# Kernel optimization log

Measured on AMD Instinct MI355X. Metric: run time of the kernel, lower is better.

## Reference

```python
import jax, jax.numpy as jnp
import numpy as np

EPS = 1e-6
H = 12  # heads

def layernorm(x, alpha, bias):
    # Faithful to source: unbiased std (ddof=1) and division by (std + eps)
    mean = jnp.mean(x, axis=-1, keepdims=True)
    std = jnp.std(x, axis=-1, ddof=1, keepdims=True)
    return alpha * (x - mean) / (std + EPS) + bias

def setup_inputs() -> dict:
    key = jax.random.key(0)
    ks = jax.random.split(key, 8)
    B, S, D, F = 2, 2048, 768, 3072
    w_scale = 0.02  # keep activations in a sane range
    return {
        "x": jax.random.normal(ks[0], (B, S, D), dtype=jnp.float32),
        "src_mask": jnp.ones((B, 1, 1, S), dtype=jnp.int32),
        "wq": jax.random.normal(ks[1], (D, D), dtype=jnp.float32) * w_scale,
        "wk": jax.random.normal(ks[2], (D, D), dtype=jnp.float32) * w_scale,
        "wv": jax.random.normal(ks[3], (D, D), dtype=jnp.float32) * w_scale,
        "wo": jax.random.normal(ks[4], (D, D), dtype=jnp.float32) * w_scale,
        "w1": jax.random.normal(ks[5], (D, F), dtype=jnp.float32) * w_scale,
        "b1": jnp.zeros((F,), dtype=jnp.float32),
        "w2": jax.random.normal(ks[6], (F, D), dtype=jnp.float32) * w_scale,
        "b2": jnp.zeros((D,), dtype=jnp.float32),
        "ln1_alpha": jnp.ones((1,), dtype=jnp.float32),
        "ln1_bias": jnp.zeros((1,), dtype=jnp.float32),
        "ln2_alpha": jnp.ones((1,), dtype=jnp.float32),
        "ln2_bias": jnp.zeros((1,), dtype=jnp.float32),
    }

def reference(x, src_mask, wq, wk, wv, wo, w1, b1, w2, b2,
              ln1_alpha, ln1_bias, ln2_alpha, ln2_bias):
    B, S, D = x.shape
    dk = D // H
    # ---- residual 1: pre-LN self-attention ----
    t = layernorm(x, ln1_alpha, ln1_bias)
    q = (t @ wq).reshape(B, S, H, dk).transpose(0, 2, 1, 3)  # [B,H,S,dk]
    k = (t @ wk).reshape(B, S, H, dk).transpose(0, 2, 1, 3)
    v = (t @ wv).reshape(B, S, H, dk).transpose(0, 2, 1, 3)
    scores = jnp.einsum('bhqd,bhkd->bhqk', q, k) / jnp.sqrt(jnp.float32(dk))
    # Faithful to source quirk: masked positions are SET to 1e-9 (not -inf)
    scores = jnp.where(src_mask == 0, jnp.float32(1e-9), scores)
    attn = jax.nn.softmax(scores, axis=-1)
    o = jnp.einsum('bhqk,bhkd->bhqd', attn, v)
    o = o.transpose(0, 2, 1, 3).reshape(B, S, D) @ wo
    x = x + o
    # ---- residual 2: pre-LN FFN ----
    t = layernorm(x, ln2_alpha, ln2_bias)
    ffn = jax.nn.relu(t @ w1 + b1) @ w2 + b2
    return x + ffn
```

## Files before the change

### kernel.cpp

```cpp
#include <hip/hip_runtime.h>

typedef float f32x4 __attribute__((ext_vector_type(4)));
typedef __bf16 bf16x8 __attribute__((ext_vector_type(8)));

__device__ __forceinline__ unsigned short f2bf(float f) {
    union { float f; unsigned u; } v; v.f = f;
    unsigned r = v.u + 0x7fffu + ((v.u >> 16) & 1u);
    return (unsigned short)(r >> 16);
}

#define AS1 __attribute__((address_space(1)))
#define AS3 __attribute__((address_space(3)))
__device__ __forceinline__ void async16(const void* g, void* l) {
    __builtin_amdgcn_global_load_lds((AS1 void*)g, (AS3 void*)l, 16, 0, 0);
}

__device__ __forceinline__ void sync_lds() {
    asm volatile("s_waitcnt lgkmcnt(0)\n\ts_barrier" ::: "memory");
}

#define SWZ4(r) ((((r) & 3) ^ (((r) >> 2) & 3)))

__global__ void transpose_cvt(const float* __restrict__ W, unsigned short* __restrict__ Wt,
                              int K, int N) {
    __shared__ float tile[32][33];
    int n0 = blockIdx.x * 32, k0 = blockIdx.y * 32;
    int tx = threadIdx.x, ty = threadIdx.y;
#pragma unroll
    for (int i = 0; i < 32; i += 8)
        tile[ty + i][tx] = W[(size_t)(k0 + ty + i) * N + n0 + tx];
    __syncthreads();
#pragma unroll
    for (int i = 0; i < 32; i += 8)
        Wt[(size_t)(n0 + ty + i) * K + k0 + tx] = f2bf(tile[tx][ty + i]);
}

__global__ __launch_bounds__(256) void ln_kernel(const float* __restrict__ x,
                                                 unsigned short* __restrict__ t,
                                                 const float* __restrict__ alpha,
                                                 const float* __restrict__ bias) {
    const int row = blockIdx.x;
    const float* xr = x + (size_t)row * 768;
    float v[3], sum = 0.f, ss = 0.f;
#pragma unroll
    for (int i = 0; i < 3; i++) {
        v[i] = xr[threadIdx.x + 256 * i];
        sum += v[i]; ss += v[i] * v[i];
    }
#pragma unroll
    for (int off = 32; off; off >>= 1) {
        sum += __shfl_down(sum, off);
        ss  += __shfl_down(ss, off);
    }
    __shared__ float s1[4], s2[4];
    int wid = threadIdx.x >> 6, lane = threadIdx.x & 63;
    if (lane == 0) { s1[wid] = sum; s2[wid] = ss; }
    __syncthreads();
    if (threadIdx.x == 0) {
        float a = 0.f, b = 0.f;
#pragma unroll
        for (int i = 0; i < 4; i++) { a += s1[i]; b += s2[i]; }
        s1[0] = a; s2[0] = b;
    }
    __syncthreads();
    sum = s1[0]; ss = s2[0];
    float mean = sum * (1.f / 768.f);
    float var = (ss - sum * mean) * (1.f / 767.f);
    float sc = alpha[0] / (sqrtf(fmaxf(var, 0.f)) + 1e-6f);
    float bs = bias[0];
#pragma unroll
    for (int i = 0; i < 3; i++)
        t[(size_t)row * 768 + threadIdx.x + 256 * i] = f2bf(sc * (v[i] - mean) + bs);
}

template <int MODE>
__global__ __launch_bounds__(256, 3) void gemm_bt(
    const unsigned short* __restrict__ A, const unsigned short* __restrict__ Bt,
    int M, int N, int K, const float* __restrict__ bias,
    const float* __restrict__ res, void* __restrict__ outp) {
    __shared__ __align__(16) unsigned short As[2][128 * 32];
    __shared__ __align__(16) unsigned short Bs[2][128 * 32];
    const int tid = threadIdx.x;
    const int lane = tid & 63, w = tid >> 6;
    const int wm = w & 1, wn = w >> 1;
    const int m0 = blockIdx.y * 128, n0 = blockIdx.x * 128;
    const int quad = lane >> 4, l16 = lane & 15;

    const int r0 = tid >> 2, g0 = tid & 3;
    const int r1 = r0 + 64, g1 = g0;
    const unsigned short* gA0 = A  + (size_t)(m0 + r0) * K + g0 * 8;
    const unsigned short* gA1 = A  + (size_t)(m0 + r1) * K + g1 * 8;
    const unsigned short* gB0 = Bt + (size_t)(n0 + r0) * K + g0 * 8;
    const unsigned short* gB1 = Bt + (size_t)(n0 + r1) * K + g1 * 8;
    const int wA0 = r0 * 32 + ((g0 ^ SWZ4(r0)) * 8);
    const int wA1 = r1 * 32 + ((g1 ^ SWZ4(r1)) * 8);

    f32x4 acc[4][4];
    const f32x4 z = {0.f, 0.f, 0.f, 0.f};
#pragma unroll
    for (int mt = 0; mt < 4; mt++)
#pragma unroll
        for (int nt = 0; nt < 4; nt++) acc[mt][nt] = z;

    bf16x8 ra0 = *(const bf16x8*)gA0, ra1 = *(const bf16x8*)gA1;
    bf16x8 rb0 = *(const bf16x8*)gB0, rb1 = *(const bf16x8*)gB1;
    gA0 += 32; gA1 += 32; gB0 += 32; gB1 += 32;

    const int nK = K >> 5;
    for (int kt = 0; kt < nK; ++kt) {
        unsigned short* Ac = As[kt & 1];
        unsigned short* Bc = Bs[kt & 1];
        *(bf16x8*)&Ac[wA0] = ra0; *(bf16x8*)&Ac[wA1] = ra1;
        *(bf16x8*)&Bc[wA0] = rb0; *(bf16x8*)&Bc[wA1] = rb1;
        if (kt + 1 < nK) {
            ra0 = *(const bf16x8*)gA0; ra1 = *(const bf16x8*)gA1;
            rb0 = *(const bf16x8*)gB0; rb1 = *(const bf16x8*)gB1;
            gA0 += 32; gA1 += 32; gB0 += 32; gB1 += 32;
        }
        sync_lds();
        bf16x8 af[4], bf[4];
#pragma unroll
        for (int mt = 0; mt < 4; mt++) {
            int r = 64 * wm + 16 * mt + l16;
            af[mt] = *(const bf16x8*)&Ac[r * 32 + ((quad ^ SWZ4(r)) * 8)];
        }
#pragma unroll
        for (int nt = 0; nt < 4; nt++) {
            int r = 64 * wn + 16 * nt + l16;
            bf[nt] = *(const bf16x8*)&Bc[r * 32 + ((quad ^ SWZ4(r)) * 8)];
        }
#pragma unroll
        for (int mt = 0; mt < 4; mt++)
#pragma unroll
            for (int nt = 0; nt < 4; nt++)
                acc[mt][nt] = __builtin_amdgcn_mfma_f32_16x16x32_bf16(af[mt], bf[nt], acc[mt][nt], 0, 0, 0);
    }

#pragma unroll
    for (int mt = 0; mt < 4; mt++) {
#pragma unroll
        for (int nt = 0; nt < 4; nt++) {
            const int col = n0 + 64 * wn + 16 * nt + l16;
            float bv = 0.f;
            if (MODE == 1 || MODE == 3) bv = bias[col];
#pragma unroll
            for (int r = 0; r < 4; r++) {
                const int row = m0 + 64 * wm + 16 * mt + quad * 4 + r;
                const size_t idx = (size_t)row * N + col;
                const float v = acc[mt][nt][r];
                if (MODE == 0) ((unsigned short*)outp)[idx] = f2bf(v);
                else if (MODE == 1) ((unsigned short*)outp)[idx] = f2bf(fmaxf(v + bv, 0.f));
                else if (MODE == 2) ((float*)outp)[idx] = v + res[idx];
                else ((float*)outp)[idx] = v + bv + res[idx];
            }
        }
    }
}

template <int MODE>
__global__ __launch_bounds__(256, 3) void gemm64_bt(
    const unsigned short* __restrict__ A, const unsigned short* __restrict__ Bt,
    int M, int N, int K, const float* __restrict__ bias,
    const float* __restrict__ res, void* __restrict__ outp) {
    __shared__ __align__(16) unsigned short As[2][64 * 64];
    __shared__ __align__(16) unsigned short Bs[2][64 * 64];
    const int tid = threadIdx.x;
    const int lane = tid & 63, w = tid >> 6;
    const int m0 = blockIdx.y * 64, n0 = blockIdx.x * 64;
    const int quad = lane >> 4, l16 = lane & 15;

    const int r0 = tid >> 3, g0 = tid & 7;
    const int r1 = r0 + 32, g1 = g0;
    const unsigned short* gA0 = A  + (size_t)(m0 + r0) * K + g0 * 8;
    const unsigned short* gA1 = A  + (size_t)(m0 + r1) * K + g1 * 8;
    const unsigned short* gB0 = Bt + (size_t)(n0 + r0) * K + g0 * 8;
    const unsigned short* gB1 = Bt + (size_t)(n0 + r1) * K + g1 * 8;
    const int wA0 = r0 * 64 + ((g0 ^ (r0 & 7)) * 8);
    const int wA1 = r1 * 64 + ((g1 ^ (r1 & 7)) * 8);

    f32x4 acc[4];
    const f32x4 z = {0.f, 0.f, 0.f, 0.f};
#pragma unroll
    for (int nt = 0; nt < 4; nt++) acc[nt] = z;

    bf16x8 ra0 = *(const bf16x8*)gA0, ra1 = *(const bf16x8*)gA1;
    bf16x8 rb0 = *(const bf16x8*)gB0, rb1 = *(const bf16x8*)gB1;
    gA0 += 64; gA1 += 64; gB0 += 64; gB1 += 64;

    const int nK = K >> 6;
    for (int kt = 0; kt < nK; ++kt) {
        unsigned short* Ac = As[kt & 1];
        unsigned short* Bc = Bs[kt & 1];
        *(bf16x8*)&Ac[wA0] = ra0; *(bf16x8*)&Ac[wA1] = ra1;
        *(bf16x8*)&Bc[wA0] = rb0; *(bf16x8*)&Bc[wA1] = rb1;
        if (kt + 1 < nK) {
            ra0 = *(const bf16x8*)gA0; ra1 = *(const bf16x8*)gA1;
            rb0 = *(const bf16x8*)gB0; rb1 = *(const bf16x8*)gB1;
            gA0 += 64; gA1 += 64; gB0 += 64; gB1 += 64;
        }
        sync_lds();
        const int ra = 16 * w + l16;
        bf16x8 af0 = *(const bf16x8*)&Ac[ra * 64 + (((0 + quad) ^ (ra & 7)) * 8)];
        bf16x8 af1 = *(const bf16x8*)&Ac[ra * 64 + (((4 + quad) ^ (ra & 7)) * 8)];
#pragma unroll
        for (int nt = 0; nt < 4; nt++) {
            int rb = 16 * nt + l16;
            bf16x8 bf0 = *(const bf16x8*)&Bc[rb * 64 + (((0 + quad) ^ (rb & 7)) * 8)];
            bf16x8 bf1 = *(const bf16x8*)&Bc[rb * 64 + (((4 + quad) ^ (rb & 7)) * 8)];
            acc[nt] = __builtin_amdgcn_mfma_f32_16x16x32_bf16(af0, bf0, acc[nt], 0, 0, 0);
            acc[nt] = __builtin_amdgcn_mfma_f32_16x16x32_bf16(af1, bf1, acc[nt], 0, 0, 0);
        }
    }

#pragma unroll
    for (int nt = 0; nt < 4; nt++) {
        const int col = n0 + 16 * nt + l16;
        float bv = 0.f;
        if (MODE == 1 || MODE == 3) bv = bias[col];
#pragma unroll
        for (int rr = 0; rr < 4; rr++) {
            const int row = m0 + 16 * w + quad * 4 + rr;
            const size_t idx = (size_t)row * N + col;
            const float v = acc[nt][rr];
            if (MODE == 0) ((unsigned short*)outp)[idx] = f2bf(v);
            else if (MODE == 1) ((unsigned short*)outp)[idx] = f2bf(fmaxf(v + bv, 0.f));
            else if (MODE == 2) ((float*)outp)[idx] = v + res[idx];
            else ((float*)outp)[idx] = v + bv + res[idx];
        }
    }
}

__global__ void v_transpose(const unsigned short* __restrict__ qkvc,
                            unsigned short* __restrict__ vt) {
    __shared__ unsigned short t[64][65];
    const int bh = blockIdx.y, b = bh / 12, h = bh % 12;
    const int s0 = blockIdx.x * 64;
    const int tx = threadIdx.x, ty = threadIdx.y;
#pragma unroll
    for (int i = 0; i < 64; i += 4)
        t[ty + i][tx] = qkvc[(size_t)(b * 2048 + s0 + ty + i) * 2304 + 1536 + h * 64 + tx];
    __syncthreads();
#pragma unroll
    for (int i = 0; i < 64; i += 4)
        vt[((size_t)bh * 64 + ty + i) * 2048 + s0 + tx] = t[tx][ty + i];
}

__global__ __launch_bounds__(256, 3) void flash_attn(
    const unsigned short* __restrict__ qkvc,
    const unsigned short* __restrict__ vt,
    const int* __restrict__ mask,
    unsigned short* __restrict__ attno) {
    const int bh = blockIdx.y, b = bh / 12, h = bh % 12;
    const int s0 = blockIdx.x * 64;
    __shared__ __align__(16) unsigned short UQP[4 * 16 * 136];
    __shared__ __align__(16) unsigned short Ks[128 * 64];
    __shared__ __align__(16) unsigned short Vs[64 * 128];
    __shared__ int Ms[128];
    const int tid = threadIdx.x, lane = tid & 63, w = tid >> 6;
    const int quad = lane >> 4, l16 = lane & 15;

    {
        int sl0 = (2 * w) * 64 + lane;
        int r0 = sl0 >> 3, g0 = sl0 & 7;
        int sl1 = sl0 + 64;
        int r1 = sl1 >> 3, g1 = sl1 & 7;
        async16(qkvc + (size_t)(b * 2048 + s0 + r0) * 2304 + h * 64 + ((g0 ^ (r0 & 7)) * 8),
                UQP + (2 * w) * 512);
        async16(qkvc + (size_t)(b * 2048 + s0 + r1) * 2304 + h * 64 + ((g1 ^ (r1 & 7)) * 8),
                UQP + (2 * w + 1) * 512);
    }
    __syncthreads();
    bf16x8 aQ[2];
    {
        int r = 16 * w + l16;
#pragma unroll
        for (int kk = 0; kk < 2; kk++)
            aQ[kk] = *(const bf16x8*)&UQP[r * 64 + (((kk * 4 + quad) ^ (r & 7)) * 8)];
    }
    __bf16* Ps = (__bf16*)(UQP + w * (16 * 136));

    f32x4 Oacc[4], Lacc;
    const f32x4 z = {0.f, 0.f, 0.f, 0.f};
#pragma unroll
    for (int nt = 0; nt < 4; nt++) Oacc[nt] = z;
    Lacc = z;
    bf16x8 ones;
#pragma unroll
    for (int i = 0; i < 8; i++) ones[i] = (__bf16)1.0f;

    const unsigned short* kbase = qkvc + 768;
    const unsigned short* vbase = vt + (size_t)bh * 64 * 2048;
    const float SCL = 0.125f * 1.44269504088896340736f;
    const float MSK = 1.4426950408889634e-9f;

    for (int j = 0; j < 16; j++) {
        const int k0 = j * 128;
        __syncthreads();
#pragma unroll
        for (int c = 0; c < 4; c++) {
            int sl = (4 * w + c) * 64 + lane;
            int r = sl >> 3, g = sl & 7;
            async16(kbase + (size_t)(b * 2048 + k0 + r) * 2304 + h * 64 + ((g ^ (r & 7)) * 8),
                    Ks + (4 * w + c) * 512);
        }
#pragma unroll
        for (int c = 0; c < 4; c++) {
            int sl = (4 * w + c) * 64 + lane;
            int r = sl >> 4, g = sl & 15;
            async16(vbase + (size_t)r * 2048 + k0 + ((g ^ (r & 15)) * 8),
                    Vs + (4 * w + c) * 512);
        }
        if (tid < 128) Ms[tid] = mask[b * 2048 + k0 + tid];
        __syncthreads();

        f32x4 sc[8];
#pragma unroll
        for (int nt = 0; nt < 8; nt++) {
            int rr = nt * 16 + l16;
            bf16x8 bk0 = *(const bf16x8*)&Ks[rr * 64 + (((0 + quad) ^ (rr & 7)) * 8)];
            bf16x8 bk1 = *(const bf16x8*)&Ks[rr * 64 + (((4 + quad) ^ (rr & 7)) * 8)];
            sc[nt] = __builtin_amdgcn_mfma_f32_16x16x32_bf16(aQ[0], bk0, z, 0, 0, 0);
            sc[nt] = __builtin_amdgcn_mfma_f32_16x16x32_bf16(aQ[1], bk1, sc[nt], 0, 0, 0);
        }
#pragma unroll
        for (int nt = 0; nt < 8; nt++) {
            const int msk = Ms[nt * 16 + l16];
#pragma unroll
            for (int r = 0; r < 4; r++) {
                float v = msk ? sc[nt][r] * SCL : MSK;
                sc[nt][r] = __builtin_amdgcn_exp2f(v);
            }
        }
#pragma unroll
        for (int nt = 0; nt < 8; nt++)
#pragma unroll
            for (int r = 0; r < 4; r++)
                Ps[(quad * 4 + r) * 136 + nt * 16 + l16] = (__bf16)sc[nt][r];

#pragma unroll
        for (int ktile = 0; ktile < 4; ktile++) {
            bf16x8 aP = *(const bf16x8*)&Ps[l16 * 136 + ktile * 32 + quad * 8];
            Lacc = __builtin_amdgcn_mfma_f32_16x16x32_bf16(aP, ones, Lacc, 0, 0, 0);
#pragma unroll
            for (int nt = 0; nt < 4; nt++) {
                int rr = nt * 16 + l16;
                bf16x8 bv = *(const bf16x8*)&Vs[rr * 128 + (((ktile * 4 + quad) ^ (rr & 15)) * 8)];
                Oacc[nt] = __builtin_amdgcn_mfma_f32_16x16x32_bf16(aP, bv, Oacc[nt], 0, 0, 0);
            }
        }
    }

    float inv[4];
#pragma unroll
    for (int r = 0; r < 4; r++) inv[r] = 1.0f / Lacc[r];
#pragma unroll
    for (int nt = 0; nt < 4; nt++)
#pragma unroll
        for (int r = 0; r < 4; r++) {
            const int row = s0 + 16 * w + quad * 4 + r;
            attno[(size_t)(b * 2048 + row) * 768 + h * 64 + nt * 16 + l16] =
                f2bf(Oacc[nt][r] * inv[r]);
        }
}

extern "C" void kernel_launch(void* const* d_in, const int* in_sizes, int n_in,
                              void* d_out, int out_size, void* d_ws, size_t ws_size,
                              hipStream_t stream) {
    const float* x    = (const float*)d_in[0];
    const int*   mask = (const int*)d_in[1];
    const float* wq   = (const float*)d_in[2];
    const float* wk   = (const float*)d_in[3];
    const float* wv   = (const float*)d_in[4];
    const float* wo   = (const float*)d_in[5];
    const float* w1   = (const float*)d_in[6];
    const float* b1   = (const float*)d_in[7];
    const float* w2   = (const float*)d_in[8];
    const float* b2   = (const float*)d_in[9];
    const float* ln1a = (const float*)d_in[10];
    const float* ln1b = (const float*)d_in[11];
    const float* ln2a = (const float*)d_in[12];
    const float* ln2b = (const float*)d_in[13];

    char* p = (char*)d_ws;
    auto carve = [&](size_t bytes) {
        char* q = p;
        p += (bytes + 255) & ~(size_t)255;
        return q;
    };
    unsigned short* wTqkv = (unsigned short*)carve((size_t)2304 * 768 * 2);
    unsigned short* wTo   = (unsigned short*)carve((size_t)768 * 768 * 2);
    unsigned short* wT1   = (unsigned short*)carve((size_t)3072 * 768 * 2);
    unsigned short* wT2   = (unsigned short*)carve((size_t)768 * 3072 * 2);
    unsigned short* vtb   = (unsigned short*)carve((size_t)24 * 64 * 2048 * 2);
    float*          x1    = (float*)carve((size_t)4096 * 768 * 4);
    char* unionA = carve((size_t)4096 * 768 * 2 + (size_t)4096 * 2304 * 2);
    unsigned short* t1   = (unsigned short*)unionA;
    unsigned short* qkvc = (unsigned short*)(unionA + (size_t)4096 * 768 * 2);
    unsigned short* ffnh = (unsigned short*)unionA;
    unsigned short* attno = (unsigned short*)carve((size_t)4096 * 768 * 2);
    unsigned short* t2 = attno;

    dim3 tb(32, 8);
    transpose_cvt<<<dim3(24, 24), tb, 0, stream>>>(wq, wTqkv, 768, 768);
    transpose_cvt<<<dim3(24, 24), tb, 0, stream>>>(wk, wTqkv + (size_t)768 * 768, 768, 768);
    transpose_cvt<<<dim3(24, 24), tb, 0, stream>>>(wv, wTqkv + (size_t)1536 * 768, 768, 768);
    transpose_cvt<<<dim3(24, 24), tb, 0, stream>>>(wo, wTo, 768, 768);
    transpose_cvt<<<dim3(96, 24), tb, 0, stream>>>(w1, wT1, 768, 3072);
    transpose_cvt<<<dim3(24, 96), tb, 0, stream>>>(w2, wT2, 3072, 768);

    ln_kernel<<<4096, 256, 0, stream>>>(x, t1, ln1a, ln1b);
    gemm_bt<0><<<dim3(18, 32), 256, 0, stream>>>(t1, wTqkv, 4096, 2304, 768,
                                                 nullptr, nullptr, qkvc);
    v_transpose<<<dim3(32, 24), dim3(64, 4), 0, stream>>>(qkvc, vtb);
    flash_attn<<<dim3(32, 24), 256, 0, stream>>>(qkvc, vtb, mask, attno);
    gemm64_bt<2><<<dim3(12, 64), 256, 0, stream>>>(attno, wTo, 4096, 768, 768,
                                                   nullptr, x, x1);
    ln_kernel<<<4096, 256, 0, stream>>>(x1, t2, ln2a, ln2b);
    gemm_bt<1><<<dim3(24, 32), 256, 0, stream>>>(t2, wT1, 4096, 3072, 768,
                                                 b1, nullptr, ffnh);
    gemm64_bt<3><<<dim3(12, 64), 256, 0, stream>>>(ffnh, wT2, 4096, 768, 3072,
                                                   b2, x1, (float*)d_out);
}
```

Before: 280.1 us.

## Register-prefetch next K/V tile in attention loop instead of async LDS loads

Replaces the per-iteration global_load_lds copies of K and V with register prefetching. The next tile is loaded into registers while the current tile is computed, then written to swizzled LDS at the start of the next iteration. This is meant to hide global-memory latency behind the MFMA work, at the cost of extra registers and an explicit LDS store pass. It also turns the per-element mask select into a single fma with precomputed per-column scale and offset.

Measured after the change: 281.7 us. About the same (+0.6%).

```diff
diff --git a/kernel.cpp b/kernel.cpp
--- a/kernel.cpp
+++ b/kernel.cpp
@@ -279,6 +279,28 @@
     }
     __bf16* Ps = (__bf16*)(UQP + w * (16 * 136));
 
+    const unsigned short* gk[4];
+    const unsigned short* gv[4];
+    int wk_[4], wv_[4];
+#pragma unroll
+    for (int c = 0; c < 4; c++) {
+        int u = tid + 256 * c;
+        int r = u >> 3, g = u & 7;
+        gk[c] = qkvc + (size_t)(b * 2048 + r) * 2304 + 768 + h * 64 + g * 8;
+        wk_[c] = r * 64 + ((g ^ (r & 7)) * 8);
+        int rd = u >> 4, gg = u & 15;
+        gv[c] = vt + (size_t)bh * 64 * 2048 + (size_t)rd * 2048 + gg * 8;
+        wv_[c] = rd * 128 + ((gg ^ (rd & 15)) * 8);
+    }
+    const int* mrow = mask + b * 2048 + tid;
+
+    bf16x8 pk[4], pv[4];
+#pragma unroll
+    for (int c = 0; c < 4; c++) pk[c] = *(const bf16x8*)gk[c];
+#pragma unroll
+    for (int c = 0; c < 4; c++) pv[c] = *(const bf16x8*)gv[c];
+    int pm = (tid < 128) ? mrow[0] : 0;
+
     f32x4 Oacc[4], Lacc;
     const f32x4 z = {0.f, 0.f, 0.f, 0.f};
 #pragma unroll
@@ -288,30 +310,24 @@
 #pragma unroll
     for (int i = 0; i < 8; i++) ones[i] = (__bf16)1.0f;
 
-    const unsigned short* kbase = qkvc + 768;
-    const unsigned short* vbase = vt + (size_t)bh * 64 * 2048;
     const float SCL = 0.125f * 1.44269504088896340736f;
     const float MSK = 1.4426950408889634e-9f;
 
     for (int j = 0; j < 16; j++) {
-        const int k0 = j * 128;
-        __syncthreads();
-#pragma unroll
-        for (int c = 0; c < 4; c++) {
-            int sl = (4 * w + c) * 64 + lane;
-            int r = sl >> 3, g = sl & 7;
-            async16(kbase + (size_t)(b * 2048 + k0 + r) * 2304 + h * 64 + ((g ^ (r & 7)) * 8),
-                    Ks + (4 * w + c) * 512);
-        }
-#pragma unroll
-        for (int c = 0; c < 4; c++) {
-            int sl = (4 * w + c) * 64 + lane;
-            int r = sl >> 4, g = sl & 15;
-            async16(vbase + (size_t)r * 2048 + k0 + ((g ^ (r & 15)) * 8),
-                    Vs + (4 * w + c) * 512);
-        }
-        if (tid < 128) Ms[tid] = mask[b * 2048 + k0 + tid];
-        __syncthreads();
+        sync_lds();
+#pragma unroll
+        for (int c = 0; c < 4; c++) *(bf16x8*)&Ks[wk_[c]] = pk[c];
+#pragma unroll
+        for (int c = 0; c < 4; c++) *(bf16x8*)&Vs[wv_[c]] = pv[c];
+        if (tid < 128) Ms[tid] = pm;
+        if (j + 1 < 16) {
+#pragma unroll
+            for (int c = 0; c < 4; c++) { gk[c] += 128 * 2304; pk[c] = *(const bf16x8*)gk[c]; }
+#pragma unroll
+            for (int c = 0; c < 4; c++) { gv[c] += 128; pv[c] = *(const bf16x8*)gv[c]; }
+            if (tid < 128) pm = mrow[(j + 1) * 128];
+        }
+        sync_lds();
 
         f32x4 sc[8];
 #pragma unroll
@@ -325,11 +341,11 @@
 #pragma unroll
         for (int nt = 0; nt < 8; nt++) {
             const int msk = Ms[nt * 16 + l16];
-#pragma unroll
-            for (int r = 0; r < 4; r++) {
-                float v = msk ? sc[nt][r] * SCL : MSK;
-                sc[nt][r] = __builtin_amdgcn_exp2f(v);
-            }
+            const float fs = msk ? SCL : 0.f;
+            const float ad = msk ? 0.f : MSK;
+#pragma unroll
+            for (int r = 0; r < 4; r++)
+                sc[nt][r] = __builtin_amdgcn_exp2f(fmaf(sc[nt][r], fs, ad));
         }
 #pragma unroll
         for (int nt = 0; nt < 8; nt++)
```

## Split keys across waves in flash attention and reduce partial outputs in LDS

Applied to the files above, without the earlier changes.

The flash attention kernel used to give each wave 16 query rows and have it read the whole 128-key K/V tile. Now every wave handles all 64 query rows against its own 32-key slice of the tile. This cuts the LDS reads of K and V per wave, reuses each loaded K/V fragment across four query tiles, and turns the mask-and-scale step into a single fma before exp2. In exchange it holds four times as many Q fragments and accumulators in registers, which may hurt occupancy. It also adds a final cross-wave reduction of the partial outputs and row sums through LDS, with extra barriers.

After: 301.9 us. 1.08x slower.

```diff
diff --git a/kernel.cpp b/kernel.cpp
--- a/kernel.cpp
+++ b/kernel.cpp
@@ -252,7 +252,7 @@
     unsigned short* __restrict__ attno) {
     const int bh = blockIdx.y, b = bh / 12, h = bh % 12;
     const int s0 = blockIdx.x * 64;
-    __shared__ __align__(16) unsigned short UQP[4 * 16 * 136];
+    __shared__ __align__(16) unsigned short UQP[4 * 64 * 40];
     __shared__ __align__(16) unsigned short Ks[128 * 64];
     __shared__ __align__(16) unsigned short Vs[64 * 128];
     __shared__ int Ms[128];
@@ -270,20 +270,24 @@
                 UQP + (2 * w + 1) * 512);
     }
     __syncthreads();
-    bf16x8 aQ[2];
-    {
-        int r = 16 * w + l16;
+    bf16x8 aQ[4][2];
+#pragma unroll
+    for (int mt = 0; mt < 4; mt++) {
+        int r = 16 * mt + l16;
 #pragma unroll
         for (int kk = 0; kk < 2; kk++)
-            aQ[kk] = *(const bf16x8*)&UQP[r * 64 + (((kk * 4 + quad) ^ (r & 7)) * 8)];
-    }
-    __bf16* Ps = (__bf16*)(UQP + w * (16 * 136));
-
-    f32x4 Oacc[4], Lacc;
+            aQ[mt][kk] = *(const bf16x8*)&UQP[r * 64 + (((kk * 4 + quad) ^ (r & 7)) * 8)];
+    }
+    __bf16* Ps = (__bf16*)UQP + w * (64 * 40);
+
+    f32x4 Oacc[4][4], Lacc[4];
     const f32x4 z = {0.f, 0.f, 0.f, 0.f};
 #pragma unroll
-    for (int nt = 0; nt < 4; nt++) Oacc[nt] = z;
-    Lacc = z;
+    for (int mt = 0; mt < 4; mt++) {
+        Lacc[mt] = z;
+#pragma unroll
+        for (int nt = 0; nt < 4; nt++) Oacc[mt][nt] = z;
+    }
     bf16x8 ones;
 #pragma unroll
     for (int i = 0; i < 8; i++) ones[i] = (__bf16)1.0f;
@@ -313,54 +317,80 @@
         if (tid < 128) Ms[tid] = mask[b * 2048 + k0 + tid];
         __syncthreads();
 
-        f32x4 sc[8];
-#pragma unroll
-        for (int nt = 0; nt < 8; nt++) {
-            int rr = nt * 16 + l16;
+        f32x4 sc[4][2];
+#pragma unroll
+        for (int nt = 0; nt < 2; nt++) {
+            const int rr = w * 32 + nt * 16 + l16;
             bf16x8 bk0 = *(const bf16x8*)&Ks[rr * 64 + (((0 + quad) ^ (rr & 7)) * 8)];
             bf16x8 bk1 = *(const bf16x8*)&Ks[rr * 64 + (((4 + quad) ^ (rr & 7)) * 8)];
-            sc[nt] = __builtin_amdgcn_mfma_f32_16x16x32_bf16(aQ[0], bk0, z, 0, 0, 0);
-            sc[nt] = __builtin_amdgcn_mfma_f32_16x16x32_bf16(aQ[1], bk1, sc[nt], 0, 0, 0);
-        }
-#pragma unroll
-        for (int nt = 0; nt < 8; nt++) {
-            const int msk = Ms[nt * 16 + l16];
-#pragma unroll
-            for (int r = 0; r < 4; r++) {
-                float v = msk ? sc[nt][r] * SCL : MSK;
-                sc[nt][r] = __builtin_amdgcn_exp2f(v);
+#pragma unroll
+            for (int mt = 0; mt < 4; mt++) {
+                f32x4 t0 = __builtin_amdgcn_mfma_f32_16x16x32_bf16(aQ[mt][0], bk0, z, 0, 0, 0);
+                sc[mt][nt] = __builtin_amdgcn_mfma_f32_16x16x32_bf16(aQ[mt][1], bk1, t0, 0, 0, 0);
             }
         }
 #pragma unroll
-        for (int nt = 0; nt < 8; nt++)
+        for (int nt = 0; nt < 2; nt++) {
+            const int msk = Ms[w * 32 + nt * 16 + l16];
+            const float fs = msk ? SCL : 0.f;
+            const float ad = msk ? 0.f : MSK;
+#pragma unroll
+            for (int mt = 0; mt < 4; mt++)
+#pragma unroll
+                for (int r = 0; r < 4; r++)
+                    sc[mt][nt][r] = __builtin_amdgcn_exp2f(fmaf(sc[mt][nt][r], fs, ad));
+        }
+#pragma unroll
+        for (int mt = 0; mt < 4; mt++)
+#pragma unroll
+            for (int nt = 0; nt < 2; nt++)
+#pragma unroll
+                for (int r = 0; r < 4; r++)
+                    Ps[(mt * 16 + quad * 4 + r) * 40 + nt * 16 + l16] = (__bf16)sc[mt][nt][r];
+
+#pragma unroll
+        for (int mt = 0; mt < 4; mt++) {
+            bf16x8 aP = *(const bf16x8*)&Ps[(mt * 16 + l16) * 40 + quad * 8];
+            Lacc[mt] = __builtin_amdgcn_mfma_f32_16x16x32_bf16(aP, ones, Lacc[mt], 0, 0, 0);
+#pragma unroll
+            for (int nt = 0; nt < 4; nt++) {
+                const int rr = nt * 16 + l16;
+                bf16x8 bv = *(const bf16x8*)&Vs[rr * 128 + (((w * 4 + quad) ^ (rr & 15)) * 8)];
+                Oacc[mt][nt] = __builtin_amdgcn_mfma_f32_16x16x32_bf16(aP, bv, Oacc[mt][nt], 0, 0, 0);
+            }
+        }
+    }
+
+    __syncthreads();
+    float* Osc = (float*)Ks;
+    float* Lsc = (float*)Vs;
+    if (l16 == 0) {
+#pragma unroll
+        for (int mt = 0; mt < 4; mt++)
 #pragma unroll
             for (int r = 0; r < 4; r++)
-                Ps[(quad * 4 + r) * 136 + nt * 16 + l16] = (__bf16)sc[nt][r];
-
-#pragma unroll
-        for (int ktile = 0; ktile < 4; ktile++) {
-            bf16x8 aP = *(const bf16x8*)&Ps[l16 * 136 + ktile * 32 + quad * 8];
-            Lacc = __builtin_amdgcn_mfma_f32_16x16x32_bf16(aP, ones, Lacc, 0, 0, 0);
-#pragma unroll
-            for (int nt = 0; nt < 4; nt++) {
-                int rr = nt * 16 + l16;
-                bf16x8 bv = *(const bf16x8*)&Vs[rr * 128 + (((ktile * 4 + quad) ^ (rr & 15)) * 8)];
-                Oacc[nt] = __builtin_amdgcn_mfma_f32_16x16x32_bf16(aP, bv, Oacc[nt], 0, 0, 0);
-            }
-        }
-    }
-
-    float inv[4];
-#pragma unroll
-    for (int r = 0; r < 4; r++) inv[r] = 1.0f / Lacc[r];
-#pragma unroll
-    for (int nt = 0; nt < 4; nt++)
-#pragma unroll
-        for (int r = 0; r < 4; r++) {
-            const int row = s0 + 16 * w + quad * 4 + r;
-            attno[(size_t)(b * 2048 + row) * 768 + h * 64 + nt * 16 + l16] =
-                f2bf(Oacc[nt][r] * inv[r]);
-        }
+                Lsc[w * 64 + mt * 16 + quad * 4 + r] = Lacc[mt][r];
+    }
+#pragma unroll
+    for (int mt = 0; mt < 4; mt++) {
+#pragma unroll
+        for (int nt = 0; nt < 4; nt++)
+#pragma unroll
+            for (int r = 0; r < 4; r++)
+                Osc[(w * 16 + quad * 4 + r) * 64 + nt * 16 + l16] = Oacc[mt][nt][r];
+        __syncthreads();
+#pragma unroll
+        for (int r2 = 0; r2 < 4; r2++) {
+            const int lrow = w * 4 + r2;
+            float s = Osc[lrow * 64 + lane] + Osc[1024 + lrow * 64 + lane]
+                    + Osc[2048 + lrow * 64 + lane] + Osc[3072 + lrow * 64 + lane];
+            float L = Lsc[mt * 16 + lrow] + Lsc[64 + mt * 16 + lrow]
+                    + Lsc[128 + mt * 16 + lrow] + Lsc[192 + mt * 16 + lrow];
+            const int row = s0 + mt * 16 + lrow;
+            attno[(size_t)(b * 2048 + row) * 768 + h * 64 + lane] = f2bf(s / L);
+        }
+        __syncthreads();
+    }
 }
 
 extern "C" void kernel_launch(void* const* d_in, const int* in_sizes, int n_in,
```
